# Performance work log

Hardware: AMD Instinct MI355X
Metric: run time of the kernel (lower is better)

## Reference

```python
import jax, jax.numpy as jnp
import numpy as np

B, S, N, P = 16, 1, 6, 70000
H0, W0, DS = 448, 800, 4
H, W = H0 // DS, W0 // DS          # 112, 200
BEV_SIDE = 200


def _apply_4x4(RT, xyz):
    # RT: [M,4,4], xyz: [M,P,3] -> [M,P,3]
    xyz1 = jnp.concatenate([xyz, jnp.ones_like(xyz[..., :1])], axis=-1)
    return jnp.einsum('mij,mpj->mpi', RT, xyz1)[..., :3]


def _scale_intrinsics4(K, sx, sy):
    # K: [M,3,3] pinhole intrinsics -> scaled, embedded in 4x4
    M = K.shape[0]
    K4 = jnp.tile(jnp.eye(4, dtype=K.dtype), (M, 1, 1))
    K4 = K4.at[:, 0, 0].set(K[:, 0, 0] * sx)
    K4 = K4.at[:, 1, 1].set(K[:, 1, 1] * sy)
    K4 = K4.at[:, 0, 2].set(K[:, 0, 2] * sx)
    K4 = K4.at[:, 1, 2].set(K[:, 1, 2] * sy)
    return K4


def setup_inputs() -> dict:
    rng = np.random.default_rng(0)
    pts = rng.uniform(-50.0, 50.0, size=(B, 1, 1, P, 3)).astype(np.float32)
    pts[..., 2] = rng.uniform(-2.0, 4.0, size=(B, 1, 1, P)).astype(np.float32)
    ilu = rng.uniform(0.0, 255.0, size=(B, 1, 1, P, 1)).astype(np.float32)
    pcloud = np.concatenate([pts, ilu], axis=-1)
    # extrinsics: cam-to-car pose, 6 cameras at yaw 0..300deg
    E = np.tile(np.eye(4, dtype=np.float32), (B, S, N, 1, 1))
    for n in range(N):
        a = 2.0 * np.pi * n / N
        c, s = np.cos(a), np.sin(a)
        E[:, :, n, :3, :3] = np.array([[c, -s, 0], [s, c, 0], [0, 0, 1]], np.float32)
        E[:, :, n, :3, 3] = np.array([2.0 * c, 2.0 * s, 1.5], np.float32)
    K = np.tile(np.eye(3, dtype=np.float32), (B, S, N, 1, 1))
    K[..., 0, 0] = 500.0
    K[..., 1, 1] = 500.0
    K[..., 0, 2] = W0 / 2.0
    K[..., 1, 2] = H0 / 2.0
    V = np.tile(np.eye(4, dtype=np.float32), (B, 1, 1, 1, 1))
    V[..., 0, 0] = 2.0
    V[..., 1, 1] = 2.0
    V[..., 0, 3] = 100.0
    V[..., 1, 3] = 100.0
    return {
        'pcloud': jnp.asarray(pcloud),
        'extrinsics': jnp.asarray(E),
        'intrinsics': jnp.asarray(K),
        'view': jnp.asarray(V),
        'bev_side': BEV_SIDE,
    }


def reference(pcloud, extrinsics, intrinsics, view, bev_side):
    sx = sy = 1.0 / DS
    bsn = B * S * N
    lidar_coords = pcloud[:, 0, 0, :, :3]                      # [B,P,3]
    ilu = jnp.repeat(pcloud[:, 0, 0, :, 3], N, axis=0)         # [BSN,P]
    view2 = view[:, 0, 0]                                      # [B,4,4]
    lidar_view = _apply_4x4(jnp.linalg.inv(view2), lidar_coords)
    xyz_car = jnp.repeat(lidar_view, N, axis=0)                # [BSN,P,3]
    K = intrinsics.reshape(bsn, 3, 3)
    E = extrinsics.reshape(bsn, 4, 4)
    Rt = jnp.swapaxes(E[:, :3, :3], 1, 2)
    Einv = E.at[:, :3, :3].set(Rt).at[:, :3, 3:4].set(-jnp.matmul(Rt, E[:, :3, 3:4]))
    pixel_from_car = jnp.matmul(_scale_intrinsics4(K, sx, sy), Einv)
    z = _apply_4x4(Einv, xyz_car)[:, :, 2]                     # cam-frame depth
    xyz_pixel = _apply_4x4(pixel_from_car, xyz_car)            # [BSN,P,3]
    normalizer = xyz_pixel[:, :, 2]
    xy = xyz_pixel[:, :, :2] / jnp.maximum(normalizer[..., None], 1e-6)
    x_, y_ = xy[:, :, 0], xy[:, :, 1]
    valid = ((x_ > -0.5) & (x_ < W - 0.5) & (y_ > -0.5) & (y_ < H - 0.5) & (z > 0.0)).astype(pcloud.dtype)
    depth = jnp.clip(normalizer, 0.0, bev_side / 2 - 1) * valid
    vilu = jnp.clip(ilu * valid, 0.0, 255.0)
    ym = jnp.clip(y_, 0.0, H - 1).astype(jnp.int32)
    xm = jnp.clip(x_, 0.0, W - 1).astype(jnp.int32)
    b = jnp.broadcast_to(jnp.arange(bsn)[:, None], (bsn, P))
    depth_grid = jnp.zeros((bsn, H, W), pcloud.dtype).at[b, ym, xm].set(depth)
    ilu_grid = jnp.zeros((bsn, H, W), pcloud.dtype).at[b, ym, xm].set(vilu)
    ilu_grid = jnp.log1p(ilu_grid) / np.log(256.0)
    depth_grid = depth_grid / (bev_side / 2)
    return jnp.concatenate([depth_grid[:, None], ilu_grid[:, None]], axis=1)  # [BSN,2,H,W]
```

## Files before the change

### kernel.cpp

```cpp
#include <hip/hip_runtime.h>
#include <math.h>

#define B_    16
#define N_    6
#define P_    70000
#define H_    112
#define W_    200
#define HW_   (H_ * W_)
#define BSN_  (B_ * N_)
#define HALF_ 56
#define CELLS_ (HALF_ * W_)
#define THREADS_ 1024
#define PMAIN 69632
#define PTAIL (P_ - PMAIN)


__device__ __forceinline__ float rdot4(float r0, float r1, float r2, float r3,
                                       float x, float y, float z) {
    float s = r0 * x;
    s = fmaf(r1, y, s);
    s = fmaf(r2, z, s);
    return s + r3;
}

__device__ __forceinline__ void inv4(const float* m, float* o) {
    float inv[16];
    inv[0]  =  m[5]*m[10]*m[15] - m[5]*m[11]*m[14] - m[9]*m[6]*m[15] + m[9]*m[7]*m[14] + m[13]*m[6]*m[11] - m[13]*m[7]*m[10];
    inv[4]  = -m[4]*m[10]*m[15] + m[4]*m[11]*m[14] + m[8]*m[6]*m[15] - m[8]*m[7]*m[14] - m[12]*m[6]*m[11] + m[12]*m[7]*m[10];
    inv[8]  =  m[4]*m[9]*m[15]  - m[4]*m[11]*m[13] - m[8]*m[5]*m[15] + m[8]*m[7]*m[13] + m[12]*m[5]*m[11] - m[12]*m[7]*m[9];
    inv[12] = -m[4]*m[9]*m[14]  + m[4]*m[10]*m[13] + m[8]*m[5]*m[14] - m[8]*m[6]*m[13] - m[12]*m[5]*m[10] + m[12]*m[6]*m[9];
    inv[1]  = -m[1]*m[10]*m[15] + m[1]*m[11]*m[14] + m[9]*m[2]*m[15] - m[9]*m[3]*m[14] - m[13]*m[2]*m[11] + m[13]*m[3]*m[10];
    inv[5]  =  m[0]*m[10]*m[15] - m[0]*m[11]*m[14] - m[8]*m[2]*m[15] + m[8]*m[3]*m[14] + m[12]*m[2]*m[11] - m[12]*m[3]*m[10];
    inv[9]  = -m[0]*m[9]*m[15]  + m[0]*m[11]*m[13] + m[8]*m[1]*m[15] - m[8]*m[3]*m[13] - m[12]*m[1]*m[11] + m[12]*m[3]*m[9];
    inv[13] =  m[0]*m[9]*m[14]  - m[0]*m[10]*m[13] - m[8]*m[1]*m[14] + m[8]*m[2]*m[13] + m[12]*m[1]*m[10] - m[12]*m[2]*m[9];
    inv[2]  =  m[1]*m[6]*m[15]  - m[1]*m[7]*m[14]  - m[5]*m[2]*m[15] + m[5]*m[3]*m[14] + m[13]*m[2]*m[7]  - m[13]*m[3]*m[6];
    inv[6]  = -m[0]*m[6]*m[15]  + m[0]*m[7]*m[14]  + m[4]*m[2]*m[15] - m[4]*m[3]*m[14] - m[12]*m[2]*m[7]  + m[12]*m[3]*m[6];
    inv[10] =  m[0]*m[5]*m[15]  - m[0]*m[7]*m[13]  - m[4]*m[1]*m[15] + m[4]*m[3]*m[13] + m[12]*m[1]*m[7]  - m[12]*m[3]*m[5];
    inv[14] = -m[0]*m[5]*m[14]  + m[0]*m[6]*m[13]  + m[4]*m[1]*m[14] - m[4]*m[2]*m[13] - m[12]*m[1]*m[6]  + m[12]*m[2]*m[5];
    inv[3]  = -m[1]*m[6]*m[11]  + m[1]*m[7]*m[10]  + m[5]*m[2]*m[11] - m[5]*m[3]*m[10] - m[9]*m[2]*m[7]   + m[9]*m[3]*m[6];
    inv[7]  =  m[0]*m[6]*m[11]  - m[0]*m[7]*m[10]  - m[4]*m[2]*m[11] + m[4]*m[3]*m[10] + m[8]*m[2]*m[7]   - m[8]*m[3]*m[6];
    inv[11] = -m[0]*m[5]*m[11]  + m[0]*m[7]*m[9]   + m[4]*m[1]*m[11] - m[4]*m[3]*m[9]  - m[8]*m[1]*m[7]   + m[8]*m[3]*m[5];
    inv[15] =  m[0]*m[5]*m[10]  - m[0]*m[6]*m[9]   - m[4]*m[1]*m[10] + m[4]*m[2]*m[9]  + m[8]*m[1]*m[6]   - m[8]*m[2]*m[5];
    float det = m[0]*inv[0] + m[1]*inv[4] + m[2]*inv[8] + m[3]*inv[12];
    float rdet = 1.0f / det;
    for (int i = 0; i < 16; ++i) o[i] = inv[i] * rdet;
}

__device__ __forceinline__ void cam_mats(const float* Ein, const float* Kin,
                                         float E2[4], float PFC[3][4]) {
    float Einv[4][4];
    for (int i = 0; i < 3; ++i)
        for (int j = 0; j < 3; ++j)
            Einv[i][j] = Ein[j * 4 + i];
    for (int i = 0; i < 3; ++i) {
        float s = Ein[0 * 4 + i] * Ein[0 * 4 + 3];
        s = fmaf(Ein[1 * 4 + i], Ein[1 * 4 + 3], s);
        s = fmaf(Ein[2 * 4 + i], Ein[2 * 4 + 3], s);
        Einv[i][3] = -s;
    }
    Einv[3][0] = Ein[12]; Einv[3][1] = Ein[13];
    Einv[3][2] = Ein[14]; Einv[3][3] = Ein[15];

    float K4[4][4] = {};
    K4[0][0] = Kin[0] * 0.25f;  K4[0][2] = Kin[2] * 0.25f;
    K4[1][1] = Kin[4] * 0.25f;  K4[1][2] = Kin[5] * 0.25f;
    K4[2][2] = 1.0f;            K4[3][3] = 1.0f;

    for (int i = 0; i < 3; ++i)
        for (int j = 0; j < 4; ++j) {
            float s = K4[i][0] * Einv[0][j];
            s = fmaf(K4[i][1], Einv[1][j], s);
            s = fmaf(K4[i][2], Einv[2][j], s);
            s = fmaf(K4[i][3], Einv[3][j], s);
            PFC[i][j] = s;
        }
    for (int j = 0; j < 4; ++j) E2[j] = Einv[2][j];
}


__global__ __launch_bounds__(THREADS_, 4) void k_lidar_ilp(
        const float4* __restrict__ pc, const float* __restrict__ extr,
        const float* __restrict__ intr, const float* __restrict__ view,
        float* __restrict__ out, const int* __restrict__ bev_side_p) {
    __shared__ int   win[CELLS_];
    __shared__ float sM[28];

    const int i    = blockIdx.x;
    const int xcd  = i & 7;
    const int s    = i >> 3;
    const int b    = xcd + 8 * (s >= 12 ? 1 : 0);
    const int c12  = s % 12;
    const int m    = b * N_ + (c12 >> 1);
    const int rlo  = (c12 & 1) * HALF_;
    const int t    = threadIdx.x;

    if (t == 0) {
        float Vi[16];
        inv4(&view[b * 16], Vi);
        for (int k = 0; k < 12; ++k) sM[k] = Vi[k];
    } else if (t == 64) {
        float E2[4], PFC[3][4];
        cam_mats(&extr[m * 16], &intr[m * 9], E2, PFC);
        for (int ii = 0; ii < 3; ++ii)
            for (int jj = 0; jj < 4; ++jj) sM[12 + ii * 4 + jj] = PFC[ii][jj];
        for (int jj = 0; jj < 4; ++jj) sM[24 + jj] = E2[jj];
    }
    for (int k = t; k < CELLS_; k += THREADS_) win[k] = -1;
    __syncthreads();

    const float V0 = sM[0],  V1 = sM[1],  V2 = sM[2],  V3 = sM[3];
    const float V4 = sM[4],  V5 = sM[5],  V6 = sM[6],  V7 = sM[7];
    const float V8 = sM[8],  V9 = sM[9],  V10 = sM[10], V11 = sM[11];
    const float P00 = sM[12], P01 = sM[13], P02 = sM[14], P03 = sM[15];
    const float P10 = sM[16], P11 = sM[17], P12 = sM[18], P13 = sM[19];
    const float P20 = sM[20], P21 = sM[21], P22 = sM[22], P23 = sM[23];

    const float4* pcb = pc + (size_t)b * P_;
    int c0 = -1, c1 = -1, c2 = -1, c3 = -1;

#define PROC(PT, PIDX)                                                        \
    {                                                                         \
        float lx = rdot4(V0, V1, V2,  V3,  (PT).x, (PT).y, (PT).z);           \
        float ly = rdot4(V4, V5, V6,  V7,  (PT).x, (PT).y, (PT).z);           \
        float lz = rdot4(V8, V9, V10, V11, (PT).x, (PT).y, (PT).z);           \
        float px = rdot4(P00, P01, P02, P03, lx, ly, lz);                     \
        float py = rdot4(P10, P11, P12, P13, lx, ly, lz);                     \
        float pz = rdot4(P20, P21, P22, P23, lx, ly, lz);                     \
        float denom = fmaxf(pz, 1e-6f);                                       \
        float x_ = px / denom;                                                \
        float y_ = py / denom;                                                \
        int ym = (int)fminf(fmaxf(y_, 0.0f), (float)(H_ - 1));                \
        int xm = (int)fminf(fmaxf(x_, 0.0f), (float)(W_ - 1));                \
        bool is_c = (xm == 0 || xm == W_ - 1) && (ym == 0 || ym == H_ - 1);   \
        int code = ((ym != 0) << 1) | (xm != 0);                              \
        c0 = (is_c && code == 0) ? (PIDX) : c0;                               \
        c1 = (is_c && code == 1) ? (PIDX) : c1;                               \
        c2 = (is_c && code == 2) ? (PIDX) : c2;                               \
        c3 = (is_c && code == 3) ? (PIDX) : c3;                               \
        int rr = ym - rlo;                                                    \
        if (!is_c && (unsigned)rr < (unsigned)HALF_)                          \
            atomicMax(&win[rr * W_ + xm], (PIDX));                            \
    }

    for (int base = 0; base < PMAIN; base += 4 * THREADS_) {
        float4 q0 = pcb[base + t];
        float4 q1 = pcb[base + t + THREADS_];
        float4 q2 = pcb[base + t + 2 * THREADS_];
        float4 q3 = pcb[base + t + 3 * THREADS_];
        PROC(q0, base + t)
        PROC(q1, base + t + THREADS_)
        PROC(q2, base + t + 2 * THREADS_)
        PROC(q3, base + t + 3 * THREADS_)
    }
    if (t < PTAIL) {
        float4 q = pcb[PMAIN + t];
        PROC(q, PMAIN + t)
    }
#undef PROC

    for (int d = 32; d; d >>= 1) {
        c0 = max(c0, __shfl_xor(c0, d));
        c1 = max(c1, __shfl_xor(c1, d));
        c2 = max(c2, __shfl_xor(c2, d));
        c3 = max(c3, __shfl_xor(c3, d));
    }
    if ((t & 63) == 0) {
        if (rlo == 0) {
            if (c0 >= 0) atomicMax(&win[0],   c0);
            if (c1 >= 0) atomicMax(&win[199], c1);
        } else {
            if (c2 >= 0) atomicMax(&win[(H_ - 1 - rlo) * W_ + 0],   c2);
            if (c3 >= 0) atomicMax(&win[(H_ - 1 - rlo) * W_ + 199], c3);
        }
    }
    __syncthreads();

    const float bev_half = (float)bev_side_p[0] * 0.5f;
    const float clip_hi  = bev_half - 1.0f;
    const float E20 = sM[24], E21 = sM[25], E22 = sM[26], E23 = sM[27];
    const int base0 = (m * 2) * HW_ + rlo * W_;
    for (int r = t; r < CELLS_; r += THREADS_) {
        int w = win[r];
        float depth = 0.0f, iluv = 0.0f;
        if (w >= 0) {
            float4 pt = pcb[w];
            float lx = rdot4(V0, V1, V2,  V3,  pt.x, pt.y, pt.z);
            float ly = rdot4(V4, V5, V6,  V7,  pt.x, pt.y, pt.z);
            float lz = rdot4(V8, V9, V10, V11, pt.x, pt.y, pt.z);
            float z  = rdot4(E20, E21, E22, E23, lx, ly, lz);
            float px = rdot4(P00, P01, P02, P03, lx, ly, lz);
            float py = rdot4(P10, P11, P12, P13, lx, ly, lz);
            float pz = rdot4(P20, P21, P22, P23, lx, ly, lz);
            float denom = fmaxf(pz, 1e-6f);
            float x_ = px / denom;
            float y_ = py / denom;
            bool valid = (x_ > -0.5f) && (x_ < (float)W_ - 0.5f) &&
                         (y_ > -0.5f) && (y_ < (float)H_ - 0.5f) && (z > 0.0f);
            if (valid) {
                float d = fminf(fmaxf(pz, 0.0f), clip_hi);
                depth = d / bev_half;
                float vi = fminf(fmaxf(pt.w, 0.0f), 255.0f);
                iluv = log1pf(vi) / 5.545177444479562f;
            }
        }
        out[base0 + r]       = depth;
        out[base0 + HW_ + r] = iluv;
    }
}


extern "C" void kernel_launch(void* const* d_in, const int* in_sizes, int n_in,
                              void* d_out, int out_size, void* d_ws, size_t ws_size,
                              hipStream_t stream) {
    const float4* pc  = (const float4*)d_in[0];
    const float* extr = (const float*)d_in[1];
    const float* intr = (const float*)d_in[2];
    const float* view = (const float*)d_in[3];
    const int*   bev  = (const int*)d_in[4];
    float* out = (float*)d_out;

    k_lidar_ilp<<<dim3(BSN_ * 2), dim3(THREADS_), 0, stream>>>(
        pc, extr, intr, view, out, bev);
}
```

Baseline: 46.72 us.

## Split point scatter into per-segment partial windows merged by a second kernel

Splits the 70000 points of each camera/half window into four segments, each handled by its own 512-thread block. Every block writes its shared-memory last-writer window to a workspace buffer, and a second kernel max-merges the four partials and computes depth and intensity. This raises the block count from 192 to 768 so more compute units take part in the scatter phase. In exchange it adds about 34 MB of workspace writes and reads plus a second launch, and the original single kernel is kept as a fallback when the workspace is too small.

After: 48.56 us. 3.9% more time.

```diff
diff --git a/kernel.cpp b/kernel.cpp
--- a/kernel.cpp
+++ b/kernel.cpp
@@ -10,9 +10,12 @@
 #define BSN_  (B_ * N_)
 #define HALF_ 56
 #define CELLS_ (HALF_ * W_)
-#define THREADS_ 1024
-#define PMAIN 69632
-#define PTAIL (P_ - PMAIN)
+#define NSEG  4
+#define SEGPTS (P_ / NSEG)
+#define T1_   512
+#define T2_   1024
+
+#define WS_NEED ((size_t)BSN_ * 2 * NSEG * CELLS_ * 4)
 
 
 __device__ __forceinline__ float rdot4(float r0, float r1, float r2, float r3,
@@ -78,20 +81,110 @@
 }
 
 
-__global__ __launch_bounds__(THREADS_, 4) void k_lidar_ilp(
+__global__ __launch_bounds__(T1_) void k_partial(
         const float4* __restrict__ pc, const float* __restrict__ extr,
         const float* __restrict__ intr, const float* __restrict__ view,
-        float* __restrict__ out, const int* __restrict__ bev_side_p) {
+        int* __restrict__ partial) {
     __shared__ int   win[CELLS_];
-    __shared__ float sM[28];
+    __shared__ float sM[24];
 
     const int i    = blockIdx.x;
     const int xcd  = i & 7;
-    const int s    = i >> 3;
-    const int b    = xcd + 8 * (s >= 12 ? 1 : 0);
-    const int c12  = s % 12;
-    const int m    = b * N_ + (c12 >> 1);
-    const int rlo  = (c12 & 1) * HALF_;
+    const int j    = i >> 3;
+    const int b    = xcd + 8 * (j >= 48 ? 1 : 0);
+    const int r    = j % 48;
+    const int cam  = r >> 3;
+    const int half = (r >> 2) & 1;
+    const int seg  = r & 3;
+    const int m    = b * N_ + cam;
+    const int rlo  = half * HALF_;
+    const int t    = threadIdx.x;
+
+    if (t == 0) {
+        float Vi[16];
+        inv4(&view[b * 16], Vi);
+        for (int k = 0; k < 12; ++k) sM[k] = Vi[k];
+    } else if (t == 64) {
+        float E2[4], PFC[3][4];
+        cam_mats(&extr[m * 16], &intr[m * 9], E2, PFC);
+        for (int ii = 0; ii < 3; ++ii)
+            for (int jj = 0; jj < 4; ++jj) sM[12 + ii * 4 + jj] = PFC[ii][jj];
+    }
+    for (int k = t; k < CELLS_; k += T1_) win[k] = -1;
+    __syncthreads();
+
+    const float V0 = sM[0],  V1 = sM[1],  V2 = sM[2],  V3 = sM[3];
+    const float V4 = sM[4],  V5 = sM[5],  V6 = sM[6],  V7 = sM[7];
+    const float V8 = sM[8],  V9 = sM[9],  V10 = sM[10], V11 = sM[11];
+    const float P00 = sM[12], P01 = sM[13], P02 = sM[14], P03 = sM[15];
+    const float P10 = sM[16], P11 = sM[17], P12 = sM[18], P13 = sM[19];
+    const float P20 = sM[20], P21 = sM[21], P22 = sM[22], P23 = sM[23];
+
+    const float4* pcb = pc + (size_t)b * P_;
+    int c0 = -1, c1 = -1, c2 = -1, c3 = -1;
+    const int p0 = seg * SEGPTS;
+
+    for (int p = p0 + t; p < p0 + SEGPTS; p += T1_) {
+        float4 pt = pcb[p];
+        float lx = rdot4(V0, V1, V2,  V3,  pt.x, pt.y, pt.z);
+        float ly = rdot4(V4, V5, V6,  V7,  pt.x, pt.y, pt.z);
+        float lz = rdot4(V8, V9, V10, V11, pt.x, pt.y, pt.z);
+        float px = rdot4(P00, P01, P02, P03, lx, ly, lz);
+        float py = rdot4(P10, P11, P12, P13, lx, ly, lz);
+        float pz = rdot4(P20, P21, P22, P23, lx, ly, lz);
+        float denom = fmaxf(pz, 1e-6f);
+        float x_ = px / denom;
+        float y_ = py / denom;
+        int ym = (int)fminf(fmaxf(y_, 0.0f), (float)(H_ - 1));
+        int xm = (int)fminf(fmaxf(x_, 0.0f), (float)(W_ - 1));
+        bool is_c = (xm == 0 || xm == W_ - 1) && (ym == 0 || ym == H_ - 1);
+        int code = ((ym != 0) << 1) | (xm != 0);
+        c0 = (is_c && code == 0) ? p : c0;
+        c1 = (is_c && code == 1) ? p : c1;
+        c2 = (is_c && code == 2) ? p : c2;
+        c3 = (is_c && code == 3) ? p : c3;
+        int rr = ym - rlo;
+        if (!is_c && (unsigned)rr < (unsigned)HALF_)
+            atomicMax(&win[rr * W_ + xm], p);
+    }
+    for (int d = 32; d; d >>= 1) {
+        c0 = max(c0, __shfl_xor(c0, d));
+        c1 = max(c1, __shfl_xor(c1, d));
+        c2 = max(c2, __shfl_xor(c2, d));
+        c3 = max(c3, __shfl_xor(c3, d));
+    }
+    if ((t & 63) == 0) {
+        if (half == 0) {
+            if (c0 >= 0) atomicMax(&win[0],   c0);
+            if (c1 >= 0) atomicMax(&win[199], c1);
+        } else {
+            if (c2 >= 0) atomicMax(&win[(H_ - 1 - rlo) * W_ + 0],   c2);
+            if (c3 >= 0) atomicMax(&win[(H_ - 1 - rlo) * W_ + 199], c3);
+        }
+    }
+    __syncthreads();
+
+    int* dst = partial + (size_t)(((m * 2 + half) * NSEG) + seg) * CELLS_;
+    for (int k = t; k < CELLS_; k += T1_) dst[k] = win[k];
+}
+
+
+__global__ __launch_bounds__(T2_) void k_mergefin(
+        const float4* __restrict__ pc, const int* __restrict__ partial,
+        const float* __restrict__ extr, const float* __restrict__ intr,
+        const float* __restrict__ view,
+        float* __restrict__ out, const int* __restrict__ bev_side_p) {
+    __shared__ float sM[28];
+
+    const int i    = blockIdx.x;
+    const int xcd  = i & 7;
+    const int j    = i >> 3;
+    const int b    = xcd + 8 * (j >= 12 ? 1 : 0);
+    const int r    = j % 12;
+    const int cam  = r >> 1;
+    const int half = r & 1;
+    const int m    = b * N_ + cam;
+    const int rlo  = half * HALF_;
     const int t    = threadIdx.x;
 
     if (t == 0) {
@@ -105,7 +198,76 @@
             for (int jj = 0; jj < 4; ++jj) sM[12 + ii * 4 + jj] = PFC[ii][jj];
         for (int jj = 0; jj < 4; ++jj) sM[24 + jj] = E2[jj];
     }
-    for (int k = t; k < CELLS_; k += THREADS_) win[k] = -1;
+    __syncthreads();
+
+    const float bev_half = (float)bev_side_p[0] * 0.5f;
+    const float clip_hi  = bev_half - 1.0f;
+    const float4* pcb = pc + (size_t)b * P_;
+    const int* pp = partial + (size_t)((m * 2 + half) * NSEG) * CELLS_;
+    const int base0 = (m * 2) * HW_ + rlo * W_;
+
+    for (int rr = t; rr < CELLS_; rr += T2_) {
+        int wv = max(max(pp[rr], pp[CELLS_ + rr]),
+                     max(pp[2 * CELLS_ + rr], pp[3 * CELLS_ + rr]));
+        float depth = 0.0f, iluv = 0.0f;
+        if (wv >= 0) {
+            float4 pt = pcb[wv];
+            float lx = rdot4(sM[0],  sM[1],  sM[2],  sM[3],  pt.x, pt.y, pt.z);
+            float ly = rdot4(sM[4],  sM[5],  sM[6],  sM[7],  pt.x, pt.y, pt.z);
+            float lz = rdot4(sM[8],  sM[9],  sM[10], sM[11], pt.x, pt.y, pt.z);
+            float z  = rdot4(sM[24], sM[25], sM[26], sM[27], lx, ly, lz);
+            float px = rdot4(sM[12], sM[13], sM[14], sM[15], lx, ly, lz);
+            float py = rdot4(sM[16], sM[17], sM[18], sM[19], lx, ly, lz);
+            float pz = rdot4(sM[20], sM[21], sM[22], sM[23], lx, ly, lz);
+            float denom = fmaxf(pz, 1e-6f);
+            float x_ = px / denom;
+            float y_ = py / denom;
+            bool valid = (x_ > -0.5f) && (x_ < (float)W_ - 0.5f) &&
+                         (y_ > -0.5f) && (y_ < (float)H_ - 0.5f) && (z > 0.0f);
+            if (valid) {
+                float d = fminf(fmaxf(pz, 0.0f), clip_hi);
+                depth = d / bev_half;
+                float vi = fminf(fmaxf(pt.w, 0.0f), 255.0f);
+                iluv = log1pf(vi) / 5.545177444479562f;
+            }
+        }
+        out[base0 + rr]       = depth;
+        out[base0 + HW_ + rr] = iluv;
+    }
+}
+
+
+#define PMAIN 69632
+#define PTAIL (P_ - PMAIN)
+
+__global__ __launch_bounds__(1024, 4) void k_lidar_ilp(
+        const float4* __restrict__ pc, const float* __restrict__ extr,
+        const float* __restrict__ intr, const float* __restrict__ view,
+        float* __restrict__ out, const int* __restrict__ bev_side_p) {
+    __shared__ int   win[CELLS_];
+    __shared__ float sM[28];
+
+    const int i    = blockIdx.x;
+    const int xcd  = i & 7;
+    const int s    = i >> 3;
+    const int b    = xcd + 8 * (s >= 12 ? 1 : 0);
+    const int c12  = s % 12;
+    const int m    = b * N_ + (c12 >> 1);
+    const int rlo  = (c12 & 1) * HALF_;
+    const int t    = threadIdx.x;
+
+    if (t == 0) {
+        float Vi[16];
+        inv4(&view[b * 16], Vi);
+        for (int k = 0; k < 12; ++k) sM[k] = Vi[k];
+    } else if (t == 64) {
+        float E2[4], PFC[3][4];
+        cam_mats(&extr[m * 16], &intr[m * 9], E2, PFC);
+        for (int ii = 0; ii < 3; ++ii)
+            for (int jj = 0; jj < 4; ++jj) sM[12 + ii * 4 + jj] = PFC[ii][jj];
+        for (int jj = 0; jj < 4; ++jj) sM[24 + jj] = E2[jj];
+    }
+    for (int k = t; k < CELLS_; k += 1024) win[k] = -1;
     __syncthreads();
 
     const float V0 = sM[0],  V1 = sM[1],  V2 = sM[2],  V3 = sM[3];
@@ -142,15 +304,15 @@
             atomicMax(&win[rr * W_ + xm], (PIDX));                            \
     }
 
-    for (int base = 0; base < PMAIN; base += 4 * THREADS_) {
+    for (int base = 0; base < PMAIN; base += 4 * 1024) {
         float4 q0 = pcb[base + t];
-        float4 q1 = pcb[base + t + THREADS_];
-        float4 q2 = pcb[base + t + 2 * THREADS_];
-        float4 q3 = pcb[base + t + 3 * THREADS_];
+        float4 q1 = pcb[base + t + 1024];
+        float4 q2 = pcb[base + t + 2 * 1024];
+        float4 q3 = pcb[base + t + 3 * 1024];
         PROC(q0, base + t)
-        PROC(q1, base + t + THREADS_)
-        PROC(q2, base + t + 2 * THREADS_)
-        PROC(q3, base + t + 3 * THREADS_)
+        PROC(q1, base + t + 1024)
+        PROC(q2, base + t + 2 * 1024)
+        PROC(q3, base + t + 3 * 1024)
     }
     if (t < PTAIL) {
         float4 q = pcb[PMAIN + t];
@@ -179,7 +341,7 @@
     const float clip_hi  = bev_half - 1.0f;
     const float E20 = sM[24], E21 = sM[25], E22 = sM[26], E23 = sM[27];
     const int base0 = (m * 2) * HW_ + rlo * W_;
-    for (int r = t; r < CELLS_; r += THREADS_) {
+    for (int r = t; r < CELLS_; r += 1024) {
         int w = win[r];
         float depth = 0.0f, iluv = 0.0f;
         if (w >= 0) {
@@ -219,6 +381,14 @@
     const int*   bev  = (const int*)d_in[4];
     float* out = (float*)d_out;
 
-    k_lidar_ilp<<<dim3(BSN_ * 2), dim3(THREADS_), 0, stream>>>(
-        pc, extr, intr, view, out, bev);
-}
+    if (ws_size >= WS_NEED) {
+        int* partial = (int*)d_ws;
+        k_partial<<<dim3(BSN_ * 2 * NSEG), dim3(T1_), 0, stream>>>(
+            pc, extr, intr, view, partial);
+        k_mergefin<<<dim3(BSN_ * 2), dim3(T2_), 0, stream>>>(
+            pc, partial, extr, intr, view, out, bev);
+    } else {
+        k_lidar_ilp<<<dim3(BSN_ * 2), dim3(1024), 0, stream>>>(
+            pc, extr, intr, view, out, bev);
+    }
+}
```

## Software-pipeline point loads and skip divisions for far-corner points

Applied to the files above, without the earlier changes.

Adds register double-buffering: the next group of four float4 points is loaded before the current group is processed, with a sched_barrier to keep the loads early. Points that clearly fall outside the image on both axes are detected by comparing against the scaled denominator and go straight to per-thread corner trackers, skipping the two divisions. The corner tracking is reduced to two registers per half-block, and the min-waves launch bound hint is removed. This raises register pressure from holding two groups of points, which may lower occupancy.

Result: faster. 42.59 us (-8.8%).

```diff
diff --git a/kernel.cpp b/kernel.cpp
--- a/kernel.cpp
+++ b/kernel.cpp
@@ -11,6 +11,7 @@
 #define HALF_ 56
 #define CELLS_ (HALF_ * W_)
 #define THREADS_ 1024
+#define GRP   (4 * THREADS_)
 #define PMAIN 69632
 #define PTAIL (P_ - PMAIN)
 
@@ -78,7 +79,7 @@
 }
 
 
-__global__ __launch_bounds__(THREADS_, 4) void k_lidar_ilp(
+__global__ __launch_bounds__(THREADS_) void k_lidar_pipe(
         const float4* __restrict__ pc, const float* __restrict__ extr,
         const float* __restrict__ intr, const float* __restrict__ view,
         float* __restrict__ out, const int* __restrict__ bev_side_p) {
@@ -91,7 +92,8 @@
     const int b    = xcd + 8 * (s >= 12 ? 1 : 0);
     const int c12  = s % 12;
     const int m    = b * N_ + (c12 >> 1);
-    const int rlo  = (c12 & 1) * HALF_;
+    const int half = c12 & 1;
+    const int rlo  = half * HALF_;
     const int t    = threadIdx.x;
 
     if (t == 0) {
@@ -116,7 +118,7 @@
     const float P20 = sM[20], P21 = sM[21], P22 = sM[22], P23 = sM[23];
 
     const float4* pcb = pc + (size_t)b * P_;
-    int c0 = -1, c1 = -1, c2 = -1, c3 = -1;
+    int cA = -1, cB = -1;
 
 #define PROC(PT, PIDX)                                                        \
     {                                                                         \
@@ -127,30 +129,55 @@
         float py = rdot4(P10, P11, P12, P13, lx, ly, lz);                     \
         float pz = rdot4(P20, P21, P22, P23, lx, ly, lz);                     \
         float denom = fmaxf(pz, 1e-6f);                                       \
-        float x_ = px / denom;                                                \
-        float y_ = py / denom;                                                \
-        int ym = (int)fminf(fmaxf(y_, 0.0f), (float)(H_ - 1));                \
-        int xm = (int)fminf(fmaxf(x_, 0.0f), (float)(W_ - 1));                \
-        bool is_c = (xm == 0 || xm == W_ - 1) && (ym == 0 || ym == H_ - 1);   \
-        int code = ((ym != 0) << 1) | (xm != 0);                              \
-        c0 = (is_c && code == 0) ? (PIDX) : c0;                               \
-        c1 = (is_c && code == 1) ? (PIDX) : c1;                               \
-        c2 = (is_c && code == 2) ? (PIDX) : c2;                               \
-        c3 = (is_c && code == 3) ? (PIDX) : c3;                               \
-        int rr = ym - rlo;                                                    \
-        if (!is_c && (unsigned)rr < (unsigned)HALF_)                          \
-            atomicMax(&win[rr * W_ + xm], (PIDX));                            \
-    }
-
-    for (int base = 0; base < PMAIN; base += 4 * THREADS_) {
-        float4 q0 = pcb[base + t];
-        float4 q1 = pcb[base + t + THREADS_];
-        float4 q2 = pcb[base + t + 2 * THREADS_];
-        float4 q3 = pcb[base + t + 3 * THREADS_];
-        PROC(q0, base + t)
-        PROC(q1, base + t + THREADS_)
-        PROC(q2, base + t + 2 * THREADS_)
-        PROC(q3, base + t + 3 * THREADS_)
+        bool x0 = (px <= 0.99f  * denom);                                     \
+        bool x1 = (px >= 201.0f * denom);                                     \
+        bool y0 = (py <= 0.99f  * denom);                                     \
+        bool y1 = (py >= 113.0f * denom);                                     \
+        bool yh = half ? y1 : y0;                                             \
+        cA = (x0 & yh) ? (PIDX) : cA;                                         \
+        cB = (x1 & yh) ? (PIDX) : cB;                                         \
+        if (!((x0 | x1) & (y0 | y1))) {                                       \
+            float x_ = px / denom;                                            \
+            float y_ = py / denom;                                            \
+            int ym = (int)fminf(fmaxf(y_, 0.0f), (float)(H_ - 1));            \
+            int xm = (int)fminf(fmaxf(x_, 0.0f), (float)(W_ - 1));            \
+            bool is_c = (xm == 0 || xm == W_ - 1) &&                          \
+                        (ym == 0 || ym == H_ - 1);                            \
+            int rr = ym - rlo;                                                \
+            if ((unsigned)rr < (unsigned)HALF_) {                             \
+                if (is_c) {                                                   \
+                    bool right = (xm != 0);                                   \
+                    cA = (!right) ? max(cA, (PIDX)) : cA;                     \
+                    cB = ( right) ? max(cB, (PIDX)) : cB;                     \
+                } else {                                                      \
+                    atomicMax(&win[rr * W_ + xm], (PIDX));                    \
+                }                                                             \
+            }                                                                 \
+        }                                                                     \
+    }
+
+    float4 q0 = pcb[t];
+    float4 q1 = pcb[t + THREADS_];
+    float4 q2 = pcb[t + 2 * THREADS_];
+    float4 q3 = pcb[t + 3 * THREADS_];
+    for (int gbase = 0; gbase < PMAIN - GRP; gbase += GRP) {
+        float4 n0 = pcb[gbase + GRP + t];
+        float4 n1 = pcb[gbase + GRP + t + THREADS_];
+        float4 n2 = pcb[gbase + GRP + t + 2 * THREADS_];
+        float4 n3 = pcb[gbase + GRP + t + 3 * THREADS_];
+        __builtin_amdgcn_sched_barrier(0);
+        PROC(q0, gbase + t)
+        PROC(q1, gbase + t + THREADS_)
+        PROC(q2, gbase + t + 2 * THREADS_)
+        PROC(q3, gbase + t + 3 * THREADS_)
+        q0 = n0; q1 = n1; q2 = n2; q3 = n3;
+    }
+    {
+        const int gbase = PMAIN - GRP;
+        PROC(q0, gbase + t)
+        PROC(q1, gbase + t + THREADS_)
+        PROC(q2, gbase + t + 2 * THREADS_)
+        PROC(q3, gbase + t + 3 * THREADS_)
     }
     if (t < PTAIL) {
         float4 q = pcb[PMAIN + t];
@@ -159,19 +186,13 @@
 #undef PROC
 
     for (int d = 32; d; d >>= 1) {
-        c0 = max(c0, __shfl_xor(c0, d));
-        c1 = max(c1, __shfl_xor(c1, d));
-        c2 = max(c2, __shfl_xor(c2, d));
-        c3 = max(c3, __shfl_xor(c3, d));
+        cA = max(cA, __shfl_xor(cA, d));
+        cB = max(cB, __shfl_xor(cB, d));
     }
     if ((t & 63) == 0) {
-        if (rlo == 0) {
-            if (c0 >= 0) atomicMax(&win[0],   c0);
-            if (c1 >= 0) atomicMax(&win[199], c1);
-        } else {
-            if (c2 >= 0) atomicMax(&win[(H_ - 1 - rlo) * W_ + 0],   c2);
-            if (c3 >= 0) atomicMax(&win[(H_ - 1 - rlo) * W_ + 199], c3);
-        }
+        int cell0 = half ? (HALF_ - 1) * W_ : 0;
+        if (cA >= 0) atomicMax(&win[cell0],          cA);
+        if (cB >= 0) atomicMax(&win[cell0 + W_ - 1], cB);
     }
     __syncthreads();
 
@@ -219,6 +240,6 @@
     const int*   bev  = (const int*)d_in[4];
     float* out = (float*)d_out;
 
-    k_lidar_ilp<<<dim3(BSN_ * 2), dim3(THREADS_), 0, stream>>>(
+    k_lidar_pipe<<<dim3(BSN_ * 2), dim3(THREADS_), 0, stream>>>(
         pc, extr, intr, view, out, bev);
 }
```
